# Kernel optimization log

Hardware: AMD Instinct MI355X
Metric: run time of the kernel (lower is better)

## Reference

```python
import jax, jax.numpy as jnp
import numpy as np

B, T, D = 16, 4096, 1024
UNITS = 1024


def setup_inputs() -> dict:
    key = jax.random.key(0)
    ks = jax.random.split(key, 8)
    s_in = 1.0 / np.sqrt(D)
    s_u = 1.0 / np.sqrt(UNITS)
    return {
        "hidden_state": jax.random.normal(ks[0], (B, D), jnp.float32),
        "encoder_output": jax.random.normal(ks[1], (B, T, D), jnp.float32),
        "W1": jax.random.normal(ks[2], (D, UNITS), jnp.float32) * s_in,
        "b1": jnp.zeros((UNITS,), jnp.float32),
        "W2": jax.random.normal(ks[3], (D, UNITS), jnp.float32) * s_in,
        "b2": jnp.zeros((UNITS,), jnp.float32),
        "V": jax.random.normal(ks[4], (UNITS, 1), jnp.float32) * s_u,
        "bv": jnp.zeros((1,), jnp.float32),
    }


def reference(hidden_state, encoder_output, W1, b1, W2, b2, V, bv):
    # Bahdanau additive attention: score = V(tanh(W1(h) + W2(enc)))
    h_proj = hidden_state @ W1 + b1                      # [B, U]
    e_proj = jnp.einsum("btd,du->btu", encoder_output, W2) + b2  # [B, T, U]
    feat = jnp.tanh(h_proj[:, None, :] + e_proj)          # [B, T, U]
    score = feat @ V + bv                                 # [B, T, 1]
    attention_weights = jax.nn.softmax(score, axis=1)     # [B, T, 1]
    context_vector = jnp.sum(attention_weights * encoder_output, axis=1)  # [B, D]
    return context_vector, attention_weights
```

## Files before the change

### kernel.cpp

```cpp
#include <hip/hip_runtime.h>
#include <hip/hip_bf16.h>
#include <math.h>

#define B_ 16
#define T_ 4096
#define D_ 1024
#define U_ 1024
#define M_ (B_*T_)

typedef __attribute__((ext_vector_type(8))) short short8;
typedef __attribute__((ext_vector_type(4))) short short4v;
typedef __attribute__((ext_vector_type(4))) float float4v;

static __device__ __forceinline__ short f2bf(float f) {
    unsigned u = __builtin_bit_cast(unsigned, f);
    u += 0x7FFFu + ((u >> 16) & 1u);
    return (short)(u >> 16);
}
static __device__ __forceinline__ float bf2f(short s) {
    unsigned u = ((unsigned)(unsigned short)s) << 16;
    return __builtin_bit_cast(float, u);
}
static __device__ __forceinline__ float fast_tanh(float x) {
    float c = fminf(fmaxf(2.f * x, -30.f), 30.f);
    float t = __expf(c);
    return __fdividef(t - 1.f, t + 1.f);
}

#define GLLDS(GP, LP) __builtin_amdgcn_global_load_lds( \
    (const __attribute__((address_space(1))) void*)(GP), \
    (__attribute__((address_space(3))) void*)(LP), 16, 0, 0)

__global__ void prep_fused(const float* __restrict__ h, const float* __restrict__ W1,
                           const float* __restrict__ b1, const float* __restrict__ b2,
                           const float* __restrict__ W2, const float* __restrict__ enc,
                           float* __restrict__ hbp, short* __restrict__ W2T,
                           short* __restrict__ encbf) {
    int bx = blockIdx.x;
    if (bx >= 512) {
        size_t g = (size_t)(bx - 512) * 256 + threadIdx.x;
        const float4v* p = (const float4v*)(enc + g * 16);
        float4v f0 = p[0], f1 = p[1], f2 = p[2], f3 = p[3];
        short8 a, b;
        a[0]=f2bf(f0[0]); a[1]=f2bf(f0[1]); a[2]=f2bf(f0[2]); a[3]=f2bf(f0[3]);
        a[4]=f2bf(f1[0]); a[5]=f2bf(f1[1]); a[6]=f2bf(f1[2]); a[7]=f2bf(f1[3]);
        b[0]=f2bf(f2[0]); b[1]=f2bf(f2[1]); b[2]=f2bf(f2[2]); b[3]=f2bf(f2[3]);
        b[4]=f2bf(f3[0]); b[5]=f2bf(f3[1]); b[6]=f2bf(f3[2]); b[7]=f2bf(f3[3]);
        short8* q = (short8*)(encbf + g * 16);
        q[0] = a; q[1] = b;
    } else if (bx < 256) {
        int kc = bx >> 6;
        int gid = (bx & 63) * 256 + threadIdx.x;
        int b = gid >> 10, u = gid & 1023;
        const float* hr = h + b * D_ + kc * 256;
        const float* w = W1 + (size_t)(kc * 256) * U_ + u;
        float s0 = 0.f, s1 = 0.f, s2 = 0.f, s3 = 0.f;
        for (int k = 0; k < 256; k += 4) {
            s0 += hr[k+0] * w[(size_t)(k+0) * U_];
            s1 += hr[k+1] * w[(size_t)(k+1) * U_];
            s2 += hr[k+2] * w[(size_t)(k+2) * U_];
            s3 += hr[k+3] * w[(size_t)(k+3) * U_];
        }
        float s = ((s0 + s1) + (s2 + s3));
        if (kc == 0) s += b1[u] + b2[u];
        hbp[kc * 16384 + gid] = s;
    } else {
        __shared__ short t[64][65];
        int x = bx - 256;
        int k0 = (x >> 4) * 64, u0 = (x & 15) * 64;
        int tx = threadIdx.x & 63, ty = threadIdx.x >> 6;
        #pragma unroll
        for (int r = 0; r < 16; ++r) {
            int kk = ty * 16 + r;
            t[kk][tx] = f2bf(W2[(size_t)(k0 + kk) * U_ + u0 + tx]);
        }
        __syncthreads();
        #pragma unroll
        for (int r = 0; r < 16; ++r) {
            int uu = ty * 16 + r;
            W2T[(size_t)(u0 + uu) * D_ + k0 + tx] = t[tx][uu];
        }
    }
}

__global__ __launch_bounds__(512, 2) void gemm_score_8ph(
    const short* __restrict__ Abf,
    const short* __restrict__ W2T,
    const float* __restrict__ hbp,
    const float* __restrict__ V,
    float* __restrict__ scorepart)
{
    __shared__ __align__(16) short lds[65536];

    const int tid = threadIdx.x;
    const int g = blockIdx.x;
    const int c = g & 7, q = g >> 3;
    const int ntile = q & 3;
    const int mtile = (q >> 2) * 8 + c;
    const int row0 = mtile * 256, n0 = ntile * 256;
    const int bidx = row0 >> 12;

    const int lane = tid & 63;
    const int wv = tid >> 6;
    const int wm = wv >> 2, wn = wv & 3;
    const int lm = lane & 15, quad = lane >> 4;

    const int srow = tid >> 3;
    const int lslot = (tid & 7) ^ (srow & 7);
    const short* aS = Abf + (size_t)(row0 + srow) * D_ + lslot * 8;
    const short* bS = W2T + (size_t)(n0  + srow) * D_ + lslot * 8;
    short* aD = lds + tid * 8;
    short* bD = lds + 32768 + tid * 8;

#define STG_A(kt, h, bf) do { \
    GLLDS(aS + (size_t)((h) * 128) * D_ + (kt) * 64,      aD + (bf) * 16384 + (h) * 8192); \
    GLLDS(aS + (size_t)((h) * 128 + 64) * D_ + (kt) * 64, aD + (bf) * 16384 + (h) * 8192 + 4096); \
} while (0)
#define STG_B(kt, h, bf) do { \
    GLLDS(bS + (size_t)((h) * 128) * D_ + (kt) * 64,      bD + (bf) * 16384 + (h) * 8192); \
    GLLDS(bS + (size_t)((h) * 128 + 64) * D_ + (kt) * 64, bD + (bf) * 16384 + (h) * 8192 + 4096); \
} while (0)
#define LDS_RD(off) (*(const short8*)(lds + (off)))
#define MFMA(a, b, c) __builtin_amdgcn_mfma_f32_16x16x32_bf16((a), (b), (c), 0, 0, 0)

    const int aB0 = (wm * 128 + lm) * 64 + (quad ^ (lm & 7)) * 8;
    const int aB1 = aB0 ^ 32;
    const int bB0 = 32768 + (wn * 64 + lm) * 64 + (quad ^ (lm & 7)) * 8;
    const int bB1 = bB0 ^ 32;

    float4v acc[8][4] = {};
    short8 Af[4][2], Bf[4][2];

    STG_A(0, 0, 0); STG_A(0, 1, 0); STG_B(0, 0, 0); STG_B(0, 1, 0);
    STG_B(1, 0, 1); STG_A(1, 0, 1); STG_B(1, 1, 1);
    asm volatile("s_waitcnt vmcnt(6)" ::: "memory");
    __builtin_amdgcn_s_barrier();
    __builtin_amdgcn_sched_barrier(0);

    for (int t = 0; t < 16; ++t) {
        const int buf = t & 1;
        const int ab = buf * 16384;
        #pragma unroll
        for (int mi = 0; mi < 4; ++mi) {
            Af[mi][0] = LDS_RD(ab + aB0 + mi * 1024);
            Af[mi][1] = LDS_RD(ab + aB1 + mi * 1024);
        }
        #pragma unroll
        for (int ni = 0; ni < 2; ++ni) {
            Bf[ni][0] = LDS_RD(ab + bB0 + ni * 1024);
            Bf[ni][1] = LDS_RD(ab + bB1 + ni * 1024);
        }
        if (t < 15) STG_A(t + 1, 1, (t + 1) & 1);
        __builtin_amdgcn_s_barrier();
        __builtin_amdgcn_s_setprio(1);
        #pragma unroll
        for (int mi = 0; mi < 4; ++mi)
            #pragma unroll
            for (int ni = 0; ni < 2; ++ni) {
                acc[mi][ni] = MFMA(Af[mi][0], Bf[ni][0], acc[mi][ni]);
                acc[mi][ni] = MFMA(Af[mi][1], Bf[ni][1], acc[mi][ni]);
            }
        __builtin_amdgcn_s_setprio(0);
        __builtin_amdgcn_s_barrier();
        #pragma unroll
        for (int ni = 0; ni < 2; ++ni) {
            Bf[2 + ni][0] = LDS_RD(ab + bB0 + (2 + ni) * 1024);
            Bf[2 + ni][1] = LDS_RD(ab + bB1 + (2 + ni) * 1024);
        }
        __builtin_amdgcn_s_barrier();
        __builtin_amdgcn_s_setprio(1);
        #pragma unroll
        for (int mi = 0; mi < 4; ++mi)
            #pragma unroll
            for (int ni = 0; ni < 2; ++ni) {
                acc[mi][2 + ni] = MFMA(Af[mi][0], Bf[2 + ni][0], acc[mi][2 + ni]);
                acc[mi][2 + ni] = MFMA(Af[mi][1], Bf[2 + ni][1], acc[mi][2 + ni]);
            }
        __builtin_amdgcn_s_setprio(0);
        __builtin_amdgcn_s_barrier();
        #pragma unroll
        for (int mi = 0; mi < 4; ++mi) {
            Af[mi][0] = LDS_RD(ab + aB0 + 4096 + mi * 1024);
            Af[mi][1] = LDS_RD(ab + aB1 + 4096 + mi * 1024);
        }
        if (t < 14) STG_B(t + 2, 0, buf);
        __builtin_amdgcn_s_barrier();
        __builtin_amdgcn_s_setprio(1);
        #pragma unroll
        for (int mi = 0; mi < 4; ++mi)
            #pragma unroll
            for (int ni = 0; ni < 2; ++ni) {
                acc[4 + mi][ni] = MFMA(Af[mi][0], Bf[ni][0], acc[4 + mi][ni]);
                acc[4 + mi][ni] = MFMA(Af[mi][1], Bf[ni][1], acc[4 + mi][ni]);
            }
        __builtin_amdgcn_s_setprio(0);
        __builtin_amdgcn_s_barrier();
        if (t < 14) { STG_A(t + 2, 0, buf); STG_B(t + 2, 1, buf); }
        __builtin_amdgcn_s_barrier();
        __builtin_amdgcn_s_setprio(1);
        #pragma unroll
        for (int mi = 0; mi < 4; ++mi)
            #pragma unroll
            for (int ni = 0; ni < 2; ++ni) {
                acc[4 + mi][2 + ni] = MFMA(Af[mi][0], Bf[2 + ni][0], acc[4 + mi][2 + ni]);
                acc[4 + mi][2 + ni] = MFMA(Af[mi][1], Bf[2 + ni][1], acc[4 + mi][2 + ni]);
            }
        __builtin_amdgcn_s_setprio(0);
        if (t < 14)      { asm volatile("s_waitcnt vmcnt(6)" ::: "memory"); }
        else if (t == 14){ asm volatile("s_waitcnt vmcnt(0)" ::: "memory"); }
        __builtin_amdgcn_s_barrier();
        __builtin_amdgcn_sched_barrier(0);
    }

    float* sbuf = (float*)lds;
    float hbv[4], Vv[4];
    #pragma unroll
    for (int ni = 0; ni < 4; ++ni) {
        int U = n0 + wn * 64 + ni * 16 + lm;
        int o = bidx * U_ + U;
        hbv[ni] = hbp[o] + hbp[16384 + o] + hbp[32768 + o] + hbp[49152 + o];
        Vv[ni]  = V[U];
    }
    #pragma unroll
    for (int mi = 0; mi < 8; ++mi) {
        #pragma unroll
        for (int r = 0; r < 4; ++r) {
            float s = 0.f;
            #pragma unroll
            for (int ni = 0; ni < 4; ++ni)
                s += fast_tanh(acc[mi][ni][r] + hbv[ni]) * Vv[ni];
            #pragma unroll
            for (int off = 1; off < 16; off <<= 1)
                s += __shfl_xor(s, off, 64);
            if (lm == 0)
                sbuf[wn * 256 + wm * 128 + mi * 16 + quad * 4 + r] = s;
        }
    }
    __syncthreads();
    if (tid < 256)
        scorepart[(size_t)ntile * M_ + row0 + tid] =
            sbuf[tid] + sbuf[256 + tid] + sbuf[512 + tid] + sbuf[768 + tid];
}

__global__ __launch_bounds__(256) void ctx_softmax(
        const float* __restrict__ scorepart,
        const float* __restrict__ bv,
        const short* __restrict__ encbf,
        float* __restrict__ out_attn,
        float* __restrict__ part)
{
    __shared__ float sm[T_];
    __shared__ float wsm[128];
    __shared__ float lacc[1024];
    __shared__ float red[8];
    const int x = blockIdx.x, tid = threadIdx.x;
    const int b = x & 15, tc = x >> 4;
    const int wvi = tid >> 6;
    const float bv0 = bv[0];
    float lmax = -1e30f;
    #pragma unroll
    for (int i = 0; i < 16; ++i) {
        int t = tid + i * 256;
        const float* sp = scorepart + (size_t)b * T_ + t;
        float s = bv0 + sp[0] + sp[M_] + sp[2 * (size_t)M_] + sp[3 * (size_t)M_];
        sm[t] = s;
        lmax = fmaxf(lmax, s);
    }
    #pragma unroll
    for (int off = 1; off < 64; off <<= 1) lmax = fmaxf(lmax, __shfl_xor(lmax, off, 64));
    if ((tid & 63) == 0) red[wvi] = lmax;
    __syncthreads();
    const float m = fmaxf(fmaxf(red[0], red[1]), fmaxf(red[2], red[3]));
    float lsum = 0.f;
    #pragma unroll
    for (int i = 0; i < 16; ++i) lsum += __expf(sm[tid + i * 256] - m);
    #pragma unroll
    for (int off = 1; off < 64; off <<= 1) lsum += __shfl_xor(lsum, off, 64);
    if ((tid & 63) == 0) red[4 + wvi] = lsum;
    __syncthreads();
    const float tot = (red[4] + red[5]) + (red[6] + red[7]);
    const float rinv = 1.f / tot;
    if ((tid >> 7) == (tc & 1)) {
        int j = tid & 127;
        int t = tc * 128 + j;
        float w = __expf(sm[t] - m) * rinv;
        wsm[j] = w;
        out_attn[b * T_ + t] = w;
    }
    __syncthreads();
    const int par = tid >> 7;
    const int d0 = (tid & 127) * 8;
    const short* e0 = encbf + (size_t)(b * T_ + tc * 128 + par) * D_ + d0;
    float4v a0 = {}, a1 = {};
    #pragma unroll 4
    for (int it = 0; it < 64; ++it) {
        short8 v = *(const short8*)(e0 + (size_t)it * 2 * D_);
        float w = wsm[it * 2 + par];
        a0[0] += w * bf2f(v[0]); a0[1] += w * bf2f(v[1]);
        a0[2] += w * bf2f(v[2]); a0[3] += w * bf2f(v[3]);
        a1[0] += w * bf2f(v[4]); a1[1] += w * bf2f(v[5]);
        a1[2] += w * bf2f(v[6]); a1[3] += w * bf2f(v[7]);
    }
    if (par) {
        *(float4v*)(lacc + (tid & 127) * 8)     = a0;
        *(float4v*)(lacc + (tid & 127) * 8 + 4) = a1;
    }
    __syncthreads();
    if (!par) {
        const float* l = lacc + tid * 8;
        a0[0] += l[0]; a0[1] += l[1]; a0[2] += l[2]; a0[3] += l[3];
        a1[0] += l[4]; a1[1] += l[5]; a1[2] += l[6]; a1[3] += l[7];
        float4v* pp = (float4v*)(part + (size_t)x * 1024 + tid * 8);
        pp[0] = a0; pp[1] = a1;
    }
}

__global__ void ctx_reduce_kernel(const float* __restrict__ part, float* __restrict__ ctx) {
    int gid = blockIdx.x * 256 + threadIdx.x;
    int b = gid >> 10, d = gid & 1023;
    float s = 0.f;
    #pragma unroll
    for (int tc = 0; tc < 32; ++tc) s += part[(size_t)(tc * 16 + b) * 1024 + d];
    ctx[gid] = s;
}

extern "C" void kernel_launch(void* const* d_in, const int* in_sizes, int n_in,
                              void* d_out, int out_size, void* d_ws, size_t ws_size,
                              hipStream_t stream) {
    const float* h   = (const float*)d_in[0];
    const float* enc = (const float*)d_in[1];
    const float* W1  = (const float*)d_in[2];
    const float* b1  = (const float*)d_in[3];
    const float* W2  = (const float*)d_in[4];
    const float* b2  = (const float*)d_in[5];
    const float* V   = (const float*)d_in[6];
    const float* bv  = (const float*)d_in[7];
    float* out = (float*)d_out;
    float* ws  = (float*)d_ws;

    float* hbp       = ws;
    float* scorepart = ws + 65536;
    short* W2T   = (short*)(ws + 65536 + 524288);
    float* ctxpart   = (float*)W2T;
    short* encbf = (short*)((char*)W2T + (size_t)U_ * D_ * 2);

    prep_fused<<<16896, 256, 0, stream>>>(h, W1, b1, b2, W2, enc, hbp, W2T, encbf);
    gemm_score_8ph<<<1024, 512, 0, stream>>>(encbf, W2T, hbp, V, scorepart);
    ctx_softmax<<<512, 256, 0, stream>>>(scorepart, bv, encbf, out + 16384, ctxpart);
    ctx_reduce_kernel<<<64, 256, 0, stream>>>(ctxpart, out);
}
```

Baseline: 559.3 us.

## Make GEMM-score kernel persistent over four M-tiles with cross-tile prefetch

The score GEMM now launches 256 blocks instead of 1024, and each block loops over four 256-row M-tiles. The global-to-LDS prefetch runs straight on into the next tile's first K-steps, so pipeline fill and drain happen once per block rather than once per tile. The score-reduction buffer moves to its own shared array so the epilogue can run while next-tile data sits in the main LDS buffers. The epilogue still serializes with a vmcnt(0) wait and syncthreads per tile. 256 blocks may map unevenly onto the CU count, and the extra shared memory could affect occupancy.

After: 582.9 us. 1.04x slower.

```diff
diff --git a/kernel.cpp b/kernel.cpp
--- a/kernel.cpp
+++ b/kernel.cpp
@@ -91,14 +91,15 @@
     float* __restrict__ scorepart)
 {
     __shared__ __align__(16) short lds[65536];
+    __shared__ float sbuf[1024];
 
     const int tid = threadIdx.x;
     const int g = blockIdx.x;
-    const int c = g & 7, q = g >> 3;
-    const int ntile = q & 3;
-    const int mtile = (q >> 2) * 8 + c;
-    const int row0 = mtile * 256, n0 = ntile * 256;
-    const int bidx = row0 >> 12;
+    const int c = g & 7;
+    const int q = g >> 3;
+    const int gi = q >> 2;
+    const int nt = q & 3;
+    const int n0 = nt * 256;
 
     const int lane = tid & 63;
     const int wv = tid >> 6;
@@ -107,18 +108,17 @@
 
     const int srow = tid >> 3;
     const int lslot = (tid & 7) ^ (srow & 7);
-    const short* aS = Abf + (size_t)(row0 + srow) * D_ + lslot * 8;
-    const short* bS = W2T + (size_t)(n0  + srow) * D_ + lslot * 8;
+    const short* bS = W2T + (size_t)(n0 + srow) * D_ + lslot * 8;
     short* aD = lds + tid * 8;
     short* bD = lds + 32768 + tid * 8;
 
-#define STG_A(kt, h, bf) do { \
-    GLLDS(aS + (size_t)((h) * 128) * D_ + (kt) * 64,      aD + (bf) * 16384 + (h) * 8192); \
-    GLLDS(aS + (size_t)((h) * 128 + 64) * D_ + (kt) * 64, aD + (bf) * 16384 + (h) * 8192 + 4096); \
+#define STG_A(base, kt, hh, bf) do { \
+    GLLDS((base) + (size_t)((hh) * 128) * D_ + (kt) * 64,      aD + (bf) * 16384 + (hh) * 8192); \
+    GLLDS((base) + (size_t)((hh) * 128 + 64) * D_ + (kt) * 64, aD + (bf) * 16384 + (hh) * 8192 + 4096); \
 } while (0)
-#define STG_B(kt, h, bf) do { \
-    GLLDS(bS + (size_t)((h) * 128) * D_ + (kt) * 64,      bD + (bf) * 16384 + (h) * 8192); \
-    GLLDS(bS + (size_t)((h) * 128 + 64) * D_ + (kt) * 64, bD + (bf) * 16384 + (h) * 8192 + 4096); \
+#define STG_B(kt, hh, bf) do { \
+    GLLDS(bS + (size_t)((hh) * 128) * D_ + (kt) * 64,      bD + (bf) * 16384 + (hh) * 8192); \
+    GLLDS(bS + (size_t)((hh) * 128 + 64) * D_ + (kt) * 64, bD + (bf) * 16384 + (hh) * 8192 + 4096); \
 } while (0)
 #define LDS_RD(off) (*(const short8*)(lds + (off)))
 #define MFMA(a, b, c) __builtin_amdgcn_mfma_f32_16x16x32_bf16((a), (b), (c), 0, 0, 0)
@@ -131,115 +131,141 @@
     float4v acc[8][4] = {};
     short8 Af[4][2], Bf[4][2];
 
-    STG_A(0, 0, 0); STG_A(0, 1, 0); STG_B(0, 0, 0); STG_B(0, 1, 0);
-    STG_B(1, 0, 1); STG_A(1, 0, 1); STG_B(1, 1, 1);
+    float Vv[4];
+    #pragma unroll
+    for (int ni = 0; ni < 4; ++ni) Vv[ni] = V[n0 + wn * 64 + ni * 16 + lm];
+
+    const int mtile0 = (c << 3) + gi;
+    const ptrdiff_t subStride = (ptrdiff_t)16384 * D_;
+    const short* aS = Abf + (size_t)(mtile0 * 256 + srow) * D_ + lslot * 8;
+
+    STG_A(aS, 0, 0, 0); STG_A(aS, 0, 1, 0); STG_B(0, 0, 0); STG_B(0, 1, 0);
+    STG_B(1, 0, 1); STG_A(aS, 1, 0, 1); STG_B(1, 1, 1);
     asm volatile("s_waitcnt vmcnt(6)" ::: "memory");
     __builtin_amdgcn_s_barrier();
     __builtin_amdgcn_sched_barrier(0);
 
-    for (int t = 0; t < 16; ++t) {
-        const int buf = t & 1;
-        const int ab = buf * 16384;
-        #pragma unroll
-        for (int mi = 0; mi < 4; ++mi) {
-            Af[mi][0] = LDS_RD(ab + aB0 + mi * 1024);
-            Af[mi][1] = LDS_RD(ab + aB1 + mi * 1024);
-        }
-        #pragma unroll
-        for (int ni = 0; ni < 2; ++ni) {
-            Bf[ni][0] = LDS_RD(ab + bB0 + ni * 1024);
-            Bf[ni][1] = LDS_RD(ab + bB1 + ni * 1024);
-        }
-        if (t < 15) STG_A(t + 1, 1, (t + 1) & 1);
+    #pragma unroll 1
+    for (int s = 0; s < 4; ++s) {
+        const short* aC = aS;
+        const short* aN = (s < 3) ? (aS + subStride) : aS;
+        for (int kt = 0; kt < 16; ++kt) {
+            const int buf = kt & 1;
+            const int ab = buf * 16384;
+            #pragma unroll
+            for (int mi = 0; mi < 4; ++mi) {
+                Af[mi][0] = LDS_RD(ab + aB0 + mi * 1024);
+                Af[mi][1] = LDS_RD(ab + aB1 + mi * 1024);
+            }
+            #pragma unroll
+            for (int ni = 0; ni < 2; ++ni) {
+                Bf[ni][0] = LDS_RD(ab + bB0 + ni * 1024);
+                Bf[ni][1] = LDS_RD(ab + bB1 + ni * 1024);
+            }
+            STG_A((kt == 15 ? aN : aC), (kt + 1) & 15, 1, (kt + 1) & 1);
+            __builtin_amdgcn_s_barrier();
+            __builtin_amdgcn_s_setprio(1);
+            #pragma unroll
+            for (int mi = 0; mi < 4; ++mi)
+                #pragma unroll
+                for (int ni = 0; ni < 2; ++ni) {
+                    acc[mi][ni] = MFMA(Af[mi][0], Bf[ni][0], acc[mi][ni]);
+                    acc[mi][ni] = MFMA(Af[mi][1], Bf[ni][1], acc[mi][ni]);
+                }
+            __builtin_amdgcn_s_setprio(0);
+            __builtin_amdgcn_s_barrier();
+            #pragma unroll
+            for (int ni = 0; ni < 2; ++ni) {
+                Bf[2 + ni][0] = LDS_RD(ab + bB0 + (2 + ni) * 1024);
+                Bf[2 + ni][1] = LDS_RD(ab + bB1 + (2 + ni) * 1024);
+            }
+            __builtin_amdgcn_s_barrier();
+            __builtin_amdgcn_s_setprio(1);
+            #pragma unroll
+            for (int mi = 0; mi < 4; ++mi)
+                #pragma unroll
+                for (int ni = 0; ni < 2; ++ni) {
+                    acc[mi][2 + ni] = MFMA(Af[mi][0], Bf[2 + ni][0], acc[mi][2 + ni]);
+                    acc[mi][2 + ni] = MFMA(Af[mi][1], Bf[2 + ni][1], acc[mi][2 + ni]);
+                }
+            __builtin_amdgcn_s_setprio(0);
+            __builtin_amdgcn_s_barrier();
+            #pragma unroll
+            for (int mi = 0; mi < 4; ++mi) {
+                Af[mi][0] = LDS_RD(ab + aB0 + 4096 + mi * 1024);
+                Af[mi][1] = LDS_RD(ab + aB1 + 4096 + mi * 1024);
+            }
+            STG_B((kt + 2) & 15, 0, buf);
+            __builtin_amdgcn_s_barrier();
+            __builtin_amdgcn_s_setprio(1);
+            #pragma unroll
+            for (int mi = 0; mi < 4; ++mi)
+                #pragma unroll
+                for (int ni = 0; ni < 2; ++ni) {
+                    acc[4 + mi][ni] = MFMA(Af[mi][0], Bf[ni][0], acc[4 + mi][ni]);
+                    acc[4 + mi][ni] = MFMA(Af[mi][1], Bf[ni][1], acc[4 + mi][ni]);
+                }
+            __builtin_amdgcn_s_setprio(0);
+            __builtin_amdgcn_s_barrier();
+            STG_A((kt >= 14 ? aN : aC), (kt + 2) & 15, 0, buf);
+            STG_B((kt + 2) & 15, 1, buf);
+            __builtin_amdgcn_s_barrier();
+            __builtin_amdgcn_s_setprio(1);
+            #pragma unroll
+            for (int mi = 0; mi < 4; ++mi)
+                #pragma unroll
+                for (int ni = 0; ni < 2; ++ni) {
+                    acc[4 + mi][2 + ni] = MFMA(Af[mi][0], Bf[2 + ni][0], acc[4 + mi][2 + ni]);
+                    acc[4 + mi][2 + ni] = MFMA(Af[mi][1], Bf[2 + ni][1], acc[4 + mi][2 + ni]);
+                }
+            __builtin_amdgcn_s_setprio(0);
+            if (kt < 15) {
+                asm volatile("s_waitcnt vmcnt(6)" ::: "memory");
+                __builtin_amdgcn_s_barrier();
+                __builtin_amdgcn_sched_barrier(0);
+            }
+        }
         __builtin_amdgcn_s_barrier();
-        __builtin_amdgcn_s_setprio(1);
-        #pragma unroll
-        for (int mi = 0; mi < 4; ++mi)
-            #pragma unroll
-            for (int ni = 0; ni < 2; ++ni) {
-                acc[mi][ni] = MFMA(Af[mi][0], Bf[ni][0], acc[mi][ni]);
-                acc[mi][ni] = MFMA(Af[mi][1], Bf[ni][1], acc[mi][ni]);
-            }
-        __builtin_amdgcn_s_setprio(0);
-        __builtin_amdgcn_s_barrier();
-        #pragma unroll
-        for (int ni = 0; ni < 2; ++ni) {
-            Bf[2 + ni][0] = LDS_RD(ab + bB0 + (2 + ni) * 1024);
-            Bf[2 + ni][1] = LDS_RD(ab + bB1 + (2 + ni) * 1024);
-        }
-        __builtin_amdgcn_s_barrier();
-        __builtin_amdgcn_s_setprio(1);
-        #pragma unroll
-        for (int mi = 0; mi < 4; ++mi)
-            #pragma unroll
-            for (int ni = 0; ni < 2; ++ni) {
-                acc[mi][2 + ni] = MFMA(Af[mi][0], Bf[2 + ni][0], acc[mi][2 + ni]);
-                acc[mi][2 + ni] = MFMA(Af[mi][1], Bf[2 + ni][1], acc[mi][2 + ni]);
-            }
-        __builtin_amdgcn_s_setprio(0);
-        __builtin_amdgcn_s_barrier();
-        #pragma unroll
-        for (int mi = 0; mi < 4; ++mi) {
-            Af[mi][0] = LDS_RD(ab + aB0 + 4096 + mi * 1024);
-            Af[mi][1] = LDS_RD(ab + aB1 + 4096 + mi * 1024);
-        }
-        if (t < 14) STG_B(t + 2, 0, buf);
-        __builtin_amdgcn_s_barrier();
-        __builtin_amdgcn_s_setprio(1);
-        #pragma unroll
-        for (int mi = 0; mi < 4; ++mi)
-            #pragma unroll
-            for (int ni = 0; ni < 2; ++ni) {
-                acc[4 + mi][ni] = MFMA(Af[mi][0], Bf[ni][0], acc[4 + mi][ni]);
-                acc[4 + mi][ni] = MFMA(Af[mi][1], Bf[ni][1], acc[4 + mi][ni]);
-            }
-        __builtin_amdgcn_s_setprio(0);
-        __builtin_amdgcn_s_barrier();
-        if (t < 14) { STG_A(t + 2, 0, buf); STG_B(t + 2, 1, buf); }
-        __builtin_amdgcn_s_barrier();
-        __builtin_amdgcn_s_setprio(1);
-        #pragma unroll
-        for (int mi = 0; mi < 4; ++mi)
-            #pragma unroll
-            for (int ni = 0; ni < 2; ++ni) {
-                acc[4 + mi][2 + ni] = MFMA(Af[mi][0], Bf[2 + ni][0], acc[4 + mi][2 + ni]);
-                acc[4 + mi][2 + ni] = MFMA(Af[mi][1], Bf[2 + ni][1], acc[4 + mi][2 + ni]);
-            }
-        __builtin_amdgcn_s_setprio(0);
-        if (t < 14)      { asm volatile("s_waitcnt vmcnt(6)" ::: "memory"); }
-        else if (t == 14){ asm volatile("s_waitcnt vmcnt(0)" ::: "memory"); }
-        __builtin_amdgcn_s_barrier();
-        __builtin_amdgcn_sched_barrier(0);
-    }
-
-    float* sbuf = (float*)lds;
-    float hbv[4], Vv[4];
-    #pragma unroll
-    for (int ni = 0; ni < 4; ++ni) {
-        int U = n0 + wn * 64 + ni * 16 + lm;
-        int o = bidx * U_ + U;
-        hbv[ni] = hbp[o] + hbp[16384 + o] + hbp[32768 + o] + hbp[49152 + o];
-        Vv[ni]  = V[U];
-    }
-    #pragma unroll
-    for (int mi = 0; mi < 8; ++mi) {
-        #pragma unroll
-        for (int r = 0; r < 4; ++r) {
-            float s = 0.f;
-            #pragma unroll
-            for (int ni = 0; ni < 4; ++ni)
-                s += fast_tanh(acc[mi][ni][r] + hbv[ni]) * Vv[ni];
-            #pragma unroll
-            for (int off = 1; off < 16; off <<= 1)
-                s += __shfl_xor(s, off, 64);
-            if (lm == 0)
-                sbuf[wn * 256 + wm * 128 + mi * 16 + quad * 4 + r] = s;
-        }
-    }
-    __syncthreads();
-    if (tid < 256)
-        scorepart[(size_t)ntile * M_ + row0 + tid] =
-            sbuf[tid] + sbuf[256 + tid] + sbuf[512 + tid] + sbuf[768 + tid];
+        {
+            const int row0_s = ((s << 6) + mtile0) << 8;
+            const int bidx = row0_s >> 12;
+            float hbv[4];
+            #pragma unroll
+            for (int ni = 0; ni < 4; ++ni) {
+                int o = bidx * U_ + n0 + wn * 64 + ni * 16 + lm;
+                hbv[ni] = hbp[o] + hbp[16384 + o] + hbp[32768 + o] + hbp[49152 + o];
+            }
+            #pragma unroll
+            for (int mi = 0; mi < 8; ++mi) {
+                #pragma unroll
+                for (int r = 0; r < 4; ++r) {
+                    float sc = 0.f;
+                    #pragma unroll
+                    for (int ni = 0; ni < 4; ++ni)
+                        sc += fast_tanh(acc[mi][ni][r] + hbv[ni]) * Vv[ni];
+                    #pragma unroll
+                    for (int off = 1; off < 16; off <<= 1)
+                        sc += __shfl_xor(sc, off, 64);
+                    if (lm == 0)
+                        sbuf[wn * 256 + wm * 128 + mi * 16 + quad * 4 + r] = sc;
+                }
+            }
+            __syncthreads();
+            if (tid < 256)
+                scorepart[(size_t)nt * M_ + row0_s + tid] =
+                    sbuf[tid] + sbuf[256 + tid] + sbuf[512 + tid] + sbuf[768 + tid];
+            asm volatile("s_waitcnt vmcnt(0)" ::: "memory");
+            __syncthreads();
+            if (s < 3) {
+                #pragma unroll
+                for (int mi = 0; mi < 8; ++mi)
+                    #pragma unroll
+                    for (int ni = 0; ni < 4; ++ni)
+                        acc[mi][ni] = (float4v){0.f, 0.f, 0.f, 0.f};
+            }
+        }
+        aS += subStride;
+    }
 }
 
 __global__ __launch_bounds__(256) void ctx_softmax(
@@ -345,7 +371,7 @@
     short* encbf = (short*)((char*)W2T + (size_t)U_ * D_ * 2);
 
     prep_fused<<<16896, 256, 0, stream>>>(h, W1, b1, b2, W2, enc, hbp, W2T, encbf);
-    gemm_score_8ph<<<1024, 512, 0, stream>>>(encbf, W2T, hbp, V, scorepart);
+    gemm_score_8ph<<<256, 512, 0, stream>>>(encbf, W2T, hbp, V, scorepart);
     ctx_softmax<<<512, 256, 0, stream>>>(scorepart, bv, encbf, out + 16384, ctxpart);
     ctx_reduce_kernel<<<64, 256, 0, stream>>>(ctxpart, out);
 }
```

## Fuse encoder fp32-to-bf16 conversion into GEMM A-tile staging

Applied to the files above, without the earlier changes.

Drops the separate pass that converted the whole encoder tensor to bf16 in the prep kernel. The GEMM now loads fp32 encoder rows into registers, rounds them to bf16 and writes them to LDS, replacing the async global-to-LDS copies for the A operand. The context kernel now reads the fp32 encoder directly instead of the bf16 copy. This removes a full read-and-write pass over the large encoder tensor, but doubles the A-operand bytes the GEMM fetches, adds register pressure and conversion ALU work inside the main loop, and doubles the bytes read in the context reduction.

Measured after the change: 560.5 us. About the same (+0.2%).

```diff
diff --git a/kernel.cpp b/kernel.cpp
--- a/kernel.cpp
+++ b/kernel.cpp
@@ -17,10 +17,6 @@
     u += 0x7FFFu + ((u >> 16) & 1u);
     return (short)(u >> 16);
 }
-static __device__ __forceinline__ float bf2f(short s) {
-    unsigned u = ((unsigned)(unsigned short)s) << 16;
-    return __builtin_bit_cast(float, u);
-}
 static __device__ __forceinline__ float fast_tanh(float x) {
     float c = fminf(fmaxf(2.f * x, -30.f), 30.f);
     float t = __expf(c);
@@ -33,22 +29,10 @@
 
 __global__ void prep_fused(const float* __restrict__ h, const float* __restrict__ W1,
                            const float* __restrict__ b1, const float* __restrict__ b2,
-                           const float* __restrict__ W2, const float* __restrict__ enc,
-                           float* __restrict__ hbp, short* __restrict__ W2T,
-                           short* __restrict__ encbf) {
+                           const float* __restrict__ W2,
+                           float* __restrict__ hbp, short* __restrict__ W2T) {
     int bx = blockIdx.x;
-    if (bx >= 512) {
-        size_t g = (size_t)(bx - 512) * 256 + threadIdx.x;
-        const float4v* p = (const float4v*)(enc + g * 16);
-        float4v f0 = p[0], f1 = p[1], f2 = p[2], f3 = p[3];
-        short8 a, b;
-        a[0]=f2bf(f0[0]); a[1]=f2bf(f0[1]); a[2]=f2bf(f0[2]); a[3]=f2bf(f0[3]);
-        a[4]=f2bf(f1[0]); a[5]=f2bf(f1[1]); a[6]=f2bf(f1[2]); a[7]=f2bf(f1[3]);
-        b[0]=f2bf(f2[0]); b[1]=f2bf(f2[1]); b[2]=f2bf(f2[2]); b[3]=f2bf(f2[3]);
-        b[4]=f2bf(f3[0]); b[5]=f2bf(f3[1]); b[6]=f2bf(f3[2]); b[7]=f2bf(f3[3]);
-        short8* q = (short8*)(encbf + g * 16);
-        q[0] = a; q[1] = b;
-    } else if (bx < 256) {
+    if (bx < 256) {
         int kc = bx >> 6;
         int gid = (bx & 63) * 256 + threadIdx.x;
         int b = gid >> 10, u = gid & 1023;
@@ -84,7 +68,7 @@
 }
 
 __global__ __launch_bounds__(512, 2) void gemm_score_8ph(
-    const short* __restrict__ Abf,
+    const float* __restrict__ encf,
     const short* __restrict__ W2T,
     const float* __restrict__ hbp,
     const float* __restrict__ V,
@@ -107,19 +91,31 @@
 
     const int srow = tid >> 3;
     const int lslot = (tid & 7) ^ (srow & 7);
-    const short* aS = Abf + (size_t)(row0 + srow) * D_ + lslot * 8;
-    const short* bS = W2T + (size_t)(n0  + srow) * D_ + lslot * 8;
-    short* aD = lds + tid * 8;
+    const float* Aenc = encf + (size_t)(row0 + srow) * D_ + lslot * 8;
+    const short* bS = W2T + (size_t)(n0 + srow) * D_ + lslot * 8;
     short* bD = lds + 32768 + tid * 8;
 
-#define STG_A(kt, h, bf) do { \
-    GLLDS(aS + (size_t)((h) * 128) * D_ + (kt) * 64,      aD + (bf) * 16384 + (h) * 8192); \
-    GLLDS(aS + (size_t)((h) * 128 + 64) * D_ + (kt) * 64, aD + (bf) * 16384 + (h) * 8192 + 4096); \
-} while (0)
 #define STG_B(kt, h, bf) do { \
     GLLDS(bS + (size_t)((h) * 128) * D_ + (kt) * 64,      bD + (bf) * 16384 + (h) * 8192); \
     GLLDS(bS + (size_t)((h) * 128 + 64) * D_ + (kt) * 64, bD + (bf) * 16384 + (h) * 8192 + 4096); \
 } while (0)
+#define LDA_ISSUE(R, kt, hh) do { \
+    const float* _p0 = Aenc + (size_t)((hh) * 128) * D_ + (kt) * 64; \
+    const float* _p1 = _p0 + (size_t)64 * D_; \
+    R##0 = *(const float4v*)_p0; \
+    R##1 = *(const float4v*)(_p0 + 4); \
+    R##2 = *(const float4v*)_p1; \
+    R##3 = *(const float4v*)(_p1 + 4); \
+} while (0)
+#define LDA_WRITE(R, hh, bfi) do { \
+    short8 _w0, _w1; \
+    _w0[0]=f2bf(R##0[0]); _w0[1]=f2bf(R##0[1]); _w0[2]=f2bf(R##0[2]); _w0[3]=f2bf(R##0[3]); \
+    _w0[4]=f2bf(R##1[0]); _w0[5]=f2bf(R##1[1]); _w0[6]=f2bf(R##1[2]); _w0[7]=f2bf(R##1[3]); \
+    _w1[0]=f2bf(R##2[0]); _w1[1]=f2bf(R##2[1]); _w1[2]=f2bf(R##2[2]); _w1[3]=f2bf(R##2[3]); \
+    _w1[4]=f2bf(R##3[0]); _w1[5]=f2bf(R##3[1]); _w1[6]=f2bf(R##3[2]); _w1[7]=f2bf(R##3[3]); \
+    *(short8*)(lds + (bfi) * 16384 + (hh) * 8192 + tid * 8) = _w0; \
+    *(short8*)(lds + (bfi) * 16384 + (hh) * 8192 + 4096 + tid * 8) = _w1; \
+} while (0)
 #define LDS_RD(off) (*(const short8*)(lds + (off)))
 #define MFMA(a, b, c) __builtin_amdgcn_mfma_f32_16x16x32_bf16((a), (b), (c), 0, 0, 0)
 
@@ -130,10 +126,16 @@
 
     float4v acc[8][4] = {};
     short8 Af[4][2], Bf[4][2];
-
-    STG_A(0, 0, 0); STG_A(0, 1, 0); STG_B(0, 0, 0); STG_B(0, 1, 0);
-    STG_B(1, 0, 1); STG_A(1, 0, 1); STG_B(1, 1, 1);
-    asm volatile("s_waitcnt vmcnt(6)" ::: "memory");
+    float4v rLO0, rLO1, rLO2, rLO3;
+    float4v rHI0, rHI1, rHI2, rHI3;
+
+    STG_B(0, 0, 0); STG_B(0, 1, 0);
+    LDA_ISSUE(rLO, 0, 0); LDA_ISSUE(rHI, 0, 1);
+    STG_B(1, 0, 1); STG_B(1, 1, 1);
+    LDA_WRITE(rLO, 0, 0);
+    LDA_WRITE(rHI, 1, 0);
+    LDA_ISSUE(rLO, 1, 0);
+    asm volatile("s_waitcnt lgkmcnt(0)" ::: "memory");
     __builtin_amdgcn_s_barrier();
     __builtin_amdgcn_sched_barrier(0);
 
@@ -150,7 +152,7 @@
             Bf[ni][0] = LDS_RD(ab + bB0 + ni * 1024);
             Bf[ni][1] = LDS_RD(ab + bB1 + ni * 1024);
         }
-        if (t < 15) STG_A(t + 1, 1, (t + 1) & 1);
+        if (t < 15) LDA_ISSUE(rHI, t + 1, 1);
         __builtin_amdgcn_s_barrier();
         __builtin_amdgcn_s_setprio(1);
         #pragma unroll
@@ -195,7 +197,9 @@
             }
         __builtin_amdgcn_s_setprio(0);
         __builtin_amdgcn_s_barrier();
-        if (t < 14) { STG_A(t + 2, 0, buf); STG_B(t + 2, 1, buf); }
+        if (t < 15) LDA_WRITE(rLO, 0, (t + 1) & 1);
+        if (t < 14) { LDA_ISSUE(rLO, t + 2, 0); STG_B(t + 2, 1, buf); }
+        if (t < 15) LDA_WRITE(rHI, 1, (t + 1) & 1);
         __builtin_amdgcn_s_barrier();
         __builtin_amdgcn_s_setprio(1);
         #pragma unroll
@@ -206,8 +210,7 @@
                 acc[4 + mi][2 + ni] = MFMA(Af[mi][1], Bf[2 + ni][1], acc[4 + mi][2 + ni]);
             }
         __builtin_amdgcn_s_setprio(0);
-        if (t < 14)      { asm volatile("s_waitcnt vmcnt(6)" ::: "memory"); }
-        else if (t == 14){ asm volatile("s_waitcnt vmcnt(0)" ::: "memory"); }
+        asm volatile("s_waitcnt lgkmcnt(0)" ::: "memory");
         __builtin_amdgcn_s_barrier();
         __builtin_amdgcn_sched_barrier(0);
     }
@@ -245,7 +248,7 @@
 __global__ __launch_bounds__(256) void ctx_softmax(
         const float* __restrict__ scorepart,
         const float* __restrict__ bv,
-        const short* __restrict__ encbf,
+        const float* __restrict__ enc,
         float* __restrict__ out_attn,
         float* __restrict__ part)
 {
@@ -290,16 +293,17 @@
     __syncthreads();
     const int par = tid >> 7;
     const int d0 = (tid & 127) * 8;
-    const short* e0 = encbf + (size_t)(b * T_ + tc * 128 + par) * D_ + d0;
+    const float* e0 = enc + (size_t)(b * T_ + tc * 128 + par) * D_ + d0;
     float4v a0 = {}, a1 = {};
     #pragma unroll 4
     for (int it = 0; it < 64; ++it) {
-        short8 v = *(const short8*)(e0 + (size_t)it * 2 * D_);
+        float4v v0 = *(const float4v*)(e0 + (size_t)it * 2 * D_);
+        float4v v1 = *(const float4v*)(e0 + (size_t)it * 2 * D_ + 4);
         float w = wsm[it * 2 + par];
-        a0[0] += w * bf2f(v[0]); a0[1] += w * bf2f(v[1]);
-        a0[2] += w * bf2f(v[2]); a0[3] += w * bf2f(v[3]);
-        a1[0] += w * bf2f(v[4]); a1[1] += w * bf2f(v[5]);
-        a1[2] += w * bf2f(v[6]); a1[3] += w * bf2f(v[7]);
+        a0[0] += w * v0[0]; a0[1] += w * v0[1];
+        a0[2] += w * v0[2]; a0[3] += w * v0[3];
+        a1[0] += w * v1[0]; a1[1] += w * v1[1];
+        a1[2] += w * v1[2]; a1[3] += w * v1[3];
     }
     if (par) {
         *(float4v*)(lacc + (tid & 127) * 8)     = a0;
@@ -342,10 +346,9 @@
     float* scorepart = ws + 65536;
     short* W2T   = (short*)(ws + 65536 + 524288);
     float* ctxpart   = (float*)W2T;
-    short* encbf = (short*)((char*)W2T + (size_t)U_ * D_ * 2);
-
-    prep_fused<<<16896, 256, 0, stream>>>(h, W1, b1, b2, W2, enc, hbp, W2T, encbf);
-    gemm_score_8ph<<<1024, 512, 0, stream>>>(encbf, W2T, hbp, V, scorepart);
-    ctx_softmax<<<512, 256, 0, stream>>>(scorepart, bv, encbf, out + 16384, ctxpart);
+
+    prep_fused<<<512, 256, 0, stream>>>(h, W1, b1, b2, W2, hbp, W2T);
+    gemm_score_8ph<<<1024, 512, 0, stream>>>(enc, W2T, hbp, V, scorepart);
+    ctx_softmax<<<512, 256, 0, stream>>>(scorepart, bv, enc, out + 16384, ctxpart);
     ctx_reduce_kernel<<<64, 256, 0, stream>>>(ctxpart, out);
 }
```
